# Kernel optimization log

Hardware: AMD Instinct MI355X
Metric: run time of the kernel (lower is better)

Reference implementation:

```python
import jax, jax.numpy as jnp
import numpy as np

N, E, F_IN, HID, HEADS, G = 50000, 800000, 128, 128, 4, 512
NEG_SLOPE = 0.2


def setup_inputs() -> dict:
    key = jax.random.key(0)
    ks = jax.random.split(key, 16)
    x = jax.random.normal(ks[0], (N, F_IN), dtype=jnp.float32)
    edge_index = jax.random.randint(ks[1], (2, E), 0, N, dtype=jnp.int32)
    batch = jnp.sort(jax.random.randint(ks[2], (N,), 0, G, dtype=jnp.int32))
    s1 = 1.0 / np.sqrt(F_IN)
    s2 = 1.0 / np.sqrt(HEADS * HID)
    params = {
        "W1": jax.random.uniform(ks[3], (F_IN, HEADS * HID), jnp.float32, -s1, s1),
        "a_src1": jax.random.normal(ks[4], (HEADS, HID), jnp.float32) * s1,
        "a_dst1": jax.random.normal(ks[5], (HEADS, HID), jnp.float32) * s1,
        "b1": jnp.zeros((HEADS * HID,), jnp.float32),
        "W2": jax.random.uniform(ks[6], (HEADS * HID, HID), jnp.float32, -s2, s2),
        "a_src2": jax.random.normal(ks[7], (1, HID), jnp.float32) * s2,
        "a_dst2": jax.random.normal(ks[8], (1, HID), jnp.float32) * s2,
        "b2": jnp.zeros((HID,), jnp.float32),
        "Wl": jax.random.normal(ks[9], (HID, 1), jnp.float32) / np.sqrt(HID),
        "bl": jnp.zeros((1,), jnp.float32),
    }
    return dict(x=x, edge_index=edge_index, batch=batch, **params)


def _gat_conv(x, W, a_src, a_dst, b, src, dst, heads, out_ch):
    n = x.shape[0]
    h = (x @ W).reshape(n, heads, out_ch)                      # [N,H,C]
    asrc = jnp.sum(h * a_src, axis=-1)                          # [N,H]
    adst = jnp.sum(h * a_dst, axis=-1)                          # [N,H]
    logits = jax.nn.leaky_relu(asrc[src] + adst[dst], NEG_SLOPE)  # [E,H]
    m = jax.ops.segment_max(logits, dst, num_segments=n)        # stable softmax per dst
    e = jnp.exp(logits - m[dst])
    denom = jax.ops.segment_sum(e, dst, num_segments=n)
    alpha = e / denom[dst]                                      # [E,H]
    out = jax.ops.segment_sum(alpha[:, :, None] * h[src], dst, num_segments=n)
    return out.reshape(n, heads * out_ch) + b


def reference(x, edge_index, batch, W1, a_src1, a_dst1, b1, W2, a_src2, a_dst2, b2, Wl, bl):
    n = x.shape[0]
    loop = jnp.arange(n, dtype=edge_index.dtype)
    src = jnp.concatenate([edge_index[0], loop])  # add_self_loops=True (PyG default)
    dst = jnp.concatenate([edge_index[1], loop])
    h = _gat_conv(x, W1, a_src1, a_dst1, b1, src, dst, HEADS, HID)
    h = jax.nn.elu(h)
    h = _gat_conv(h, W2, a_src2, a_dst2, b2, src, dst, 1, HID)
    h = jax.nn.elu(h)
    # global_mean_pool
    sums = jax.ops.segment_sum(h, batch, num_segments=G)
    cnts = jax.ops.segment_sum(jnp.ones((n,), h.dtype), batch, num_segments=G)
    pooled = sums / jnp.maximum(cnts, 1.0)[:, None]
    return (pooled @ Wl + bl).squeeze()
```

## Files before the change

kernel.cpp:

```cpp
#include <hip/hip_runtime.h>
#include <math.h>

#define NEG_SLOPE 0.2f

typedef float f4 __attribute__((ext_vector_type(4)));
typedef __attribute__((ext_vector_type(8))) short short8;
typedef __attribute__((ext_vector_type(4))) float f32x4;
typedef unsigned short ushort_t;

__device__ __forceinline__ float bf2f(unsigned short s) {
    unsigned u = ((unsigned)s) << 16;
    float f; __builtin_memcpy(&f, &u, 4); return f;
}
__device__ __forceinline__ unsigned short f2bf(float f) {
    unsigned u; __builtin_memcpy(&u, &f, 4);
    u = (u + 0x7FFFu + ((u >> 16) & 1u)) >> 16;
    return (unsigned short)u;
}
__device__ __forceinline__ void gload16(const void* g, void* l) {
    __builtin_amdgcn_global_load_lds((const __attribute__((address_space(1))) void*)g,
                                     (__attribute__((address_space(3))) void*)l, 16, 0, 0);
}

__global__ void hist_kernel(const int* __restrict__ ei, int E, int Et, int* __restrict__ deg) {
    int e = blockIdx.x * blockDim.x + threadIdx.x;
    if (e >= Et) return;
    int d = (e < E) ? ei[E + e] : (e - E);
    atomicAdd(&deg[d], 1);
}

__global__ __launch_bounds__(1024) void scan_local(const int* __restrict__ deg,
                                                   int* __restrict__ off,
                                                   int* __restrict__ btot, int n) {
    __shared__ int s_w[16];
    int tid = threadIdx.x, lane = tid & 63, wv = tid >> 6;
    int i = blockIdx.x * 1024 + tid;
    int v = (i < n) ? deg[i] : 0;
    int x = v;
    #pragma unroll
    for (int d = 1; d < 64; d <<= 1) {
        int y = __shfl_up(x, d);
        if (lane >= d) x += y;
    }
    if (lane == 63) s_w[wv] = x;
    __syncthreads();
    if (tid < 16) {
        int y = s_w[tid];
        int z = y;
        #pragma unroll
        for (int d = 1; d < 16; d <<= 1) {
            int t2 = __shfl_up(z, d);
            if (tid >= d) z += t2;
        }
        if (tid == 15) btot[blockIdx.x] = z;
        s_w[tid] = z - y;
    }
    __syncthreads();
    if (i < n) off[i] = s_w[wv] + (x - v);
}

__global__ void scan_base(int* __restrict__ btot, int nb) {
    int lane = threadIdx.x;
    int v = (lane < nb) ? btot[lane] : 0;
    int x = v;
    #pragma unroll
    for (int d = 1; d < 64; d <<= 1) {
        int y = __shfl_up(x, d);
        if (lane >= d) x += y;
    }
    int total = __shfl(x, nb - 1);
    if (lane < nb) btot[lane] = x - v;
    if (lane == 0) btot[nb] = total;
}

__global__ void scan_add(const int* __restrict__ btot, int* __restrict__ off,
                         int* __restrict__ cur, const int* __restrict__ batch,
                         int* __restrict__ gcnt, int n, int nb) {
    int i = blockIdx.x * blockDim.x + threadIdx.x;
    if (i < n) {
        int o = off[i] + btot[i >> 10];
        off[i] = o;
        cur[i] = o;
        atomicAdd(&gcnt[batch[i]], 1);
    } else if (i == n) {
        off[n] = btot[nb];
    }
}

__global__ void scatter_kernel(const int* __restrict__ ei, int E, int Et,
                               int* __restrict__ cur, int* __restrict__ csr) {
    int e = blockIdx.x * blockDim.x + threadIdx.x;
    if (e >= Et) return;
    int s, d;
    if (e < E) { s = ei[e]; d = ei[E + e]; }
    else       { s = d = e - E; }
    int p = atomicAdd(&cur[d], 1);
    csr[p] = s;
}

__global__ void cast_all(const float* __restrict__ x, const float* __restrict__ W1,
                         const float* __restrict__ W2, ushort_t* __restrict__ xb,
                         ushort_t* __restrict__ W1t, ushort_t* __restrict__ W2t,
                         int n_x, int pad_x) {
    int i = blockIdx.x * blockDim.x + threadIdx.x;
    if (i < pad_x) {
        xb[i] = f2bf(i < n_x ? x[i] : 0.f);
        return;
    }
    int k = i - pad_x;
    if (k < 128 * 512) {
        int r = k >> 9, c = k & 511;
        W1t[(size_t)c * 128 + r] = f2bf(W1[k]);
        return;
    }
    k -= 128 * 512;
    if (k < 512 * 128) {
        int r = k >> 7, c = k & 127;
        W2t[(size_t)c * 512 + r] = f2bf(W2[k]);
    }
}

template<int MI, int H>
__global__ __launch_bounds__(256) void gemm_bf16(const ushort_t* __restrict__ A,
                                                 const ushort_t* __restrict__ Bt,
                                                 ushort_t* __restrict__ C,
                                                 const float* __restrict__ aw_src,
                                                 const float* __restrict__ aw_dst,
                                                 float* __restrict__ avs,
                                                 float* __restrict__ avd,
                                                 int K, int Nc) {
    constexpr int BM = MI * 32;
    constexpr int AI = MI / 2;
    __shared__ __align__(16) ushort_t As[BM * 32];
    __shared__ __align__(16) ushort_t Bs[128 * 32];
    __shared__ __align__(16) ushort_t Cs[4 * MI * 16 * 72];
    const int t = threadIdx.x, w = t >> 6, lane = t & 63;
    const int r0 = blockIdx.x * BM, c0 = blockIdx.y * 128;
    const int wr = w & 1, wc = w >> 1;

    const ushort_t* Ag = A + (size_t)(r0 + w * (BM / 4) + (lane >> 2)) * K + (lane & 3) * 8;
    const ushort_t* Bg = Bt + (size_t)(c0 + w * 32 + (lane >> 2)) * K + (lane & 3) * 8;
    ushort_t* Al = As + w * (BM / 4) * 32;
    ushort_t* Bl = Bs + w * 1024;

    f32x4 acc[MI][4] = {};
    for (int k0 = 0; k0 < K; k0 += 32) {
        __syncthreads();
        #pragma unroll
        for (int m = 0; m < AI; m++) gload16(Ag + k0 + (size_t)m * 16 * K, Al + m * 512);
        gload16(Bg + k0, Bl);
        gload16(Bg + k0 + (size_t)16 * K, Bl + 512);
        __syncthreads();
        short8 af[MI], bf[4];
        #pragma unroll
        for (int i = 0; i < MI; i++)
            af[i] = *(const short8*)(As + (wr * MI * 16 + i * 16 + (lane & 15)) * 32 + (lane >> 4) * 8);
        #pragma unroll
        for (int jj = 0; jj < 4; jj++)
            bf[jj] = *(const short8*)(Bs + (wc * 64 + jj * 16 + (lane & 15)) * 32 + (lane >> 4) * 8);
        #pragma unroll
        for (int i = 0; i < MI; i++)
            #pragma unroll
            for (int jj = 0; jj < 4; jj++)
                acc[i][jj] = __builtin_amdgcn_mfma_f32_16x16x32_bf16(af[i], bf[jj], acc[i][jj], 0, 0, 0);
    }

    const int head = c0 >> 7;
    float asc[4], adc[4];
    #pragma unroll
    for (int jj = 0; jj < 4; jj++) {
        int c = c0 + wc * 64 + jj * 16 + (lane & 15);
        asc[jj] = aw_src[c];
        adc[jj] = aw_dst[c];
    }
    #pragma unroll
    for (int i = 0; i < MI; i++) {
        #pragma unroll
        for (int r = 0; r < 4; r++) {
            float ps = 0.f, pd = 0.f;
            #pragma unroll
            for (int jj = 0; jj < 4; jj++) {
                float v = acc[i][jj][r];
                ps = fmaf(v, asc[jj], ps);
                pd = fmaf(v, adc[jj], pd);
            }
            #pragma unroll
            for (int d = 1; d < 16; d <<= 1) {
                ps += __shfl_xor(ps, d);
                pd += __shfl_xor(pd, d);
            }
            if ((lane & 15) == 0) {
                int row = r0 + wr * MI * 16 + i * 16 + (lane >> 4) * 4 + r;
                atomicAdd(&avs[(size_t)row * H + head], ps);
                atomicAdd(&avd[(size_t)row * H + head], pd);
            }
        }
    }

    ushort_t* Cw = Cs + w * (MI * 16 * 72);
    #pragma unroll
    for (int i = 0; i < MI; i++)
        #pragma unroll
        for (int jj = 0; jj < 4; jj++)
            #pragma unroll
            for (int r = 0; r < 4; r++)
                Cw[(i * 16 + (lane >> 4) * 4 + r) * 72 + jj * 16 + (lane & 15)] = f2bf(acc[i][jj][r]);
    asm volatile("s_waitcnt lgkmcnt(0)" ::: "memory");
    #pragma unroll
    for (int pass = 0; pass < MI * 2; pass++) {
        int row_l = pass * 8 + (lane >> 3);
        short8 v = *(const short8*)(Cw + row_l * 72 + (lane & 7) * 8);
        int grow = r0 + wr * MI * 16 + row_l;
        int gcol = c0 + wc * 64 + (lane & 7) * 8;
        *(short8*)(C + (size_t)grow * Nc + gcol) = v;
    }
}

template<int H, int TOT, bool OUT_BF16>
__global__ __launch_bounds__(256) void agg_kernel(const int* __restrict__ off,
                                                  const int* __restrict__ csr,
                                                  const ushort_t* __restrict__ feat,
                                                  const float* __restrict__ avs,
                                                  const float* __restrict__ avd,
                                                  const float* __restrict__ bias,
                                                  void* __restrict__ outv, int n) {
    constexpr int J = TOT / 64;
    __shared__ float s_ex[4][64 * H];
    __shared__ int   s_sv[4][64];
    int w = threadIdx.x >> 6, lane = threadIdx.x & 63;
    int dst = blockIdx.x * 4 + w;
    if (dst >= n) return;
    const int h_own = (lane * J) / (TOT / H);
    float adv[H];
    if constexpr (H == 4) {
        f4 t4 = *(const f4*)&avd[(size_t)dst * 4];
        #pragma unroll
        for (int h = 0; h < 4; h++) adv[h] = t4[h];
    } else {
        adv[0] = avd[dst];
    }
    int beg = off[dst], end = off[dst + 1];
    float den = 0.f;
    float acc[J] = {};
    float* exw = s_ex[w];
    int*   svw = s_sv[w];

    for (int b = beg; b < end; b += 64) {
        int idx = b + lane;
        bool val = idx < end;
        int sv = val ? csr[idx] : 0;
        svw[lane] = sv;
        if constexpr (H == 4) {
            f4 av = {};
            if (val) av = *(const f4*)&avs[(size_t)sv * 4];
            f4 exv;
            #pragma unroll
            for (int h = 0; h < 4; h++) {
                float l = av[h] + adv[h];
                l = l > 0.f ? l : NEG_SLOPE * l;
                exv[h] = val ? __expf(l) : 0.f;
            }
            *(f4*)&exw[lane * 4] = exv;
        } else {
            float l = (val ? avs[sv] : 0.f) + adv[0];
            l = l > 0.f ? l : NEG_SLOPE * l;
            exw[lane] = val ? __expf(l) : 0.f;
        }
        asm volatile("s_waitcnt lgkmcnt(0)" ::: "memory");
        int cnt = min(64, end - b);
        int j = 0;
        for (; j + 2 <= cnt; j += 2) {
            int   s0 = svw[j],              s1 = svw[j + 1];
            float e0 = exw[j * H + h_own],  e1 = exw[(j + 1) * H + h_own];
            den += e0 + e1;
            const ushort_t* f0 = feat + (size_t)s0 * TOT + lane * J;
            const ushort_t* f1 = feat + (size_t)s1 * TOT + lane * J;
            if constexpr (J == 8) {
                short8 v0 = *(const short8*)f0;
                short8 v1 = *(const short8*)f1;
                #pragma unroll
                for (int u = 0; u < 8; u++) acc[u] += e0 * bf2f((unsigned short)v0[u]);
                #pragma unroll
                for (int u = 0; u < 8; u++) acc[u] += e1 * bf2f((unsigned short)v1[u]);
            } else {
                unsigned v0 = *(const unsigned*)f0;
                unsigned v1 = *(const unsigned*)f1;
                acc[0] += e0 * bf2f((unsigned short)(v0 & 0xffffu));
                acc[1] += e0 * bf2f((unsigned short)(v0 >> 16));
                acc[0] += e1 * bf2f((unsigned short)(v1 & 0xffffu));
                acc[1] += e1 * bf2f((unsigned short)(v1 >> 16));
            }
        }
        if (j < cnt) {
            int   s0 = svw[j];
            float e0 = exw[j * H + h_own];
            den += e0;
            const ushort_t* f0 = feat + (size_t)s0 * TOT + lane * J;
            if constexpr (J == 8) {
                short8 v0 = *(const short8*)f0;
                #pragma unroll
                for (int u = 0; u < 8; u++) acc[u] += e0 * bf2f((unsigned short)v0[u]);
            } else {
                unsigned v0 = *(const unsigned*)f0;
                acc[0] += e0 * bf2f((unsigned short)(v0 & 0xffffu));
                acc[1] += e0 * bf2f((unsigned short)(v0 >> 16));
            }
        }
    }
    float rden = 1.f / den;
    if constexpr (OUT_BF16) {
        unsigned short ov[J];
        #pragma unroll
        for (int u = 0; u < J; u++) {
            float v = acc[u] * rden + bias[lane * J + u];
            v = v > 0.f ? v : expm1f(v);
            ov[u] = f2bf(v);
        }
        *(short8*)((ushort_t*)outv + (size_t)dst * TOT + lane * J) = *(short8*)ov;
    } else {
        float v0 = acc[0] * rden + bias[lane * 2];
        float v1 = acc[1] * rden + bias[lane * 2 + 1];
        v0 = v0 > 0.f ? v0 : expm1f(v0);
        v1 = v1 > 0.f ? v1 : expm1f(v1);
        float2 vv = make_float2(v0, v1);
        *(float2*)((float*)outv + (size_t)dst * TOT + lane * 2) = vv;
    }
}

__global__ __launch_bounds__(256) void pool_kernel(const float* __restrict__ feat,
                                                   const int* __restrict__ batch,
                                                   float* __restrict__ gsum, int n) {
    int t = threadIdx.x;
    int ch = t & 127, half = t >> 7;
    int base = blockIdx.x * 64;
    float acc = 0.f;
    int curg = -1;
    for (int k = half; k < 64; k += 2) {
        int node = base + k;
        if (node >= n) break;
        int g = batch[node];
        if (g != curg) {
            if (curg >= 0) atomicAdd(&gsum[(size_t)curg * 128 + ch], acc);
            acc = 0.f;
            curg = g;
        }
        acc += feat[(size_t)node * 128 + ch];
    }
    if (curg >= 0) atomicAdd(&gsum[(size_t)curg * 128 + ch], acc);
}

__global__ __launch_bounds__(256) void final_kernel(const float* __restrict__ gsum,
                                                    const int* __restrict__ gcnt,
                                                    const float* __restrict__ Wl,
                                                    const float* __restrict__ bl,
                                                    float* __restrict__ out, int g_total) {
    int w = threadIdx.x >> 6, lane = threadIdx.x & 63;
    int g = blockIdx.x * 4 + w;
    if (g >= g_total) return;
    float inv = 1.f / fmaxf((float)gcnt[g], 1.f);
    float p = 0.f;
    #pragma unroll
    for (int j = 0; j < 2; j++) {
        int ch = lane + 64 * j;
        p += gsum[(size_t)g * 128 + ch] * Wl[ch];
    }
    #pragma unroll
    for (int d = 32; d; d >>= 1) p += __shfl_xor(p, d);
    if (lane == 0) out[g] = p * inv + bl[0];
}

extern "C" void kernel_launch(void* const* d_in, const int* in_sizes, int n_in,
                              void* d_out, int out_size, void* d_ws, size_t ws_size,
                              hipStream_t stream) {
    const float* x   = (const float*)d_in[0];
    const int*   ei  = (const int*)d_in[1];
    const int*   bat = (const int*)d_in[2];
    const float* W1  = (const float*)d_in[3];
    const float* as1 = (const float*)d_in[4];
    const float* ad1 = (const float*)d_in[5];
    const float* b1  = (const float*)d_in[6];
    const float* W2  = (const float*)d_in[7];
    const float* as2 = (const float*)d_in[8];
    const float* ad2 = (const float*)d_in[9];
    const float* b2  = (const float*)d_in[10];
    const float* Wl  = (const float*)d_in[11];
    const float* bl  = (const float*)d_in[12];
    float* out = (float*)d_out;

    const int N    = in_sizes[0] / 128;
    const int E    = in_sizes[1] / 2;
    const int Et   = E + N;
    const int G    = 512;
    const int Mpad = (N + 127) & ~127;
    const int nb   = (N + 1023) >> 10;

    char* p = (char*)d_ws;
    auto alloc = [&](size_t bytes) { char* r = p; p += (bytes + 255) & ~(size_t)255; return r; };
    ushort_t* xb    = (ushort_t*)alloc((size_t)Mpad * 128 * 2);
    ushort_t* W1t   = (ushort_t*)alloc((size_t)512 * 128 * 2);
    ushort_t* W2t   = (ushort_t*)alloc((size_t)128 * 512 * 2);
    ushort_t* h1b   = (ushort_t*)alloc((size_t)Mpad * 512 * 2);
    ushort_t* hb    = (ushort_t*)alloc((size_t)Mpad * 512 * 2);
    ushort_t* h2b   = (ushort_t*)alloc((size_t)Mpad * 128 * 2);
    float*    feat2 = (float*)alloc((size_t)N * 128 * 4);
    float*    avs1  = (float*)alloc((size_t)Mpad * 4 * 4);
    float*    avd1  = (float*)alloc((size_t)Mpad * 4 * 4);
    float*    avs2  = (float*)alloc((size_t)Mpad * 4);
    float*    avd2  = (float*)alloc((size_t)Mpad * 4);
    float*    gsum  = (float*)alloc((size_t)G * 128 * 4);
    int*      gcnt  = (int*)alloc((size_t)G * 4);
    int*      deg   = (int*)alloc((size_t)N * 4);
    int*      off   = (int*)alloc((size_t)(N + 1) * 4);
    int*      cur   = (int*)alloc((size_t)N * 4);
    int*      btot  = (int*)alloc((size_t)64 * 4);
    int*      csr   = (int*)alloc((size_t)Et * 4);

    hipMemsetAsync(avs1, 0, (size_t)((char*)off - (char*)avs1), stream);
    hipMemsetAsync(hb + (size_t)N * 512, 0, (size_t)(Mpad - N) * 512 * 2, stream);

    hist_kernel<<<(Et + 255) / 256, 256, 0, stream>>>(ei, E, Et, deg);
    scan_local<<<nb, 1024, 0, stream>>>(deg, off, btot, N);
    scan_base<<<1, 64, 0, stream>>>(btot, nb);
    scan_add<<<(N + 256) / 256, 256, 0, stream>>>(btot, off, cur, bat, gcnt, N, nb);
    cast_all<<<((Mpad * 128 + 2 * 65536) + 255) / 256, 256, 0, stream>>>(x, W1, W2, xb, W1t, W2t,
                                                                         N * 128, Mpad * 128);
    scatter_kernel<<<(Et + 255) / 256, 256, 0, stream>>>(ei, E, Et, cur, csr);

    gemm_bf16<4, 4><<<dim3(Mpad / 128, 4), 256, 0, stream>>>(xb, W1t, h1b, as1, ad1, avs1, avd1, 128, 512);
    agg_kernel<4, 512, true><<<(N + 3) / 4, 256, 0, stream>>>(off, csr, h1b, avs1, avd1, b1, hb, N);

    gemm_bf16<2, 1><<<dim3(Mpad / 64, 1), 256, 0, stream>>>(hb, W2t, h2b, as2, ad2, avs2, avd2, 512, 128);
    agg_kernel<1, 128, false><<<(N + 3) / 4, 256, 0, stream>>>(off, csr, h2b, avs2, avd2, b2, feat2, N);

    pool_kernel<<<(N + 63) / 64, 256, 0, stream>>>(feat2, bat, gsum, N);
    final_kernel<<<(G + 3) / 4, 256, 0, stream>>>(gsum, gcnt, Wl, bl, out, G);
}
```

Before: 501.6 us.

## Quantize GEMM outputs to per-row int8 and aggregate from quantized features

The GEMMs now compute full output rows per block and quantize each row to 8-bit with a per-row scale, writing uint8 features plus a scale array in place of bf16. The aggregation kernels gather these bytes, fold the row scale into the attention weight and correct the zero-point offset with a running sum. This halves the gather traffic in the edge-bound aggregation steps, and the attention-vector atomics become plain stores. The cost is lower feature precision, which risks accuracy tolerance, plus a different GEMM tiling with smaller row tiles.

New measurement: 441.7 us. 11.9% less time.

```diff
diff --git a/kernel.cpp b/kernel.cpp
--- a/kernel.cpp
+++ b/kernel.cpp
@@ -7,6 +7,7 @@
 typedef __attribute__((ext_vector_type(8))) short short8;
 typedef __attribute__((ext_vector_type(4))) float f32x4;
 typedef unsigned short ushort_t;
+typedef unsigned char uchar_t;
 
 __device__ __forceinline__ float bf2f(unsigned short s) {
     unsigned u = ((unsigned)s) << 16;
@@ -120,66 +121,89 @@
     }
 }
 
-template<int MI, int H>
-__global__ __launch_bounds__(256) void gemm_bf16(const ushort_t* __restrict__ A,
-                                                 const ushort_t* __restrict__ Bt,
-                                                 ushort_t* __restrict__ C,
-                                                 const float* __restrict__ aw_src,
-                                                 const float* __restrict__ aw_dst,
-                                                 float* __restrict__ avs,
-                                                 float* __restrict__ avd,
-                                                 int K, int Nc) {
-    constexpr int BM = MI * 32;
-    constexpr int AI = MI / 2;
-    __shared__ __align__(16) ushort_t As[BM * 32];
-    __shared__ __align__(16) ushort_t Bs[128 * 32];
-    __shared__ __align__(16) ushort_t Cs[4 * MI * 16 * 72];
+template<int BN, int H>
+__global__ __launch_bounds__(256) void gemm_q(const ushort_t* __restrict__ A,
+                                              const ushort_t* __restrict__ Bt,
+                                              uchar_t* __restrict__ Cq,
+                                              float* __restrict__ Csc,
+                                              const float* __restrict__ aw_src,
+                                              const float* __restrict__ aw_dst,
+                                              float* __restrict__ avs,
+                                              float* __restrict__ avd,
+                                              int K) {
+    constexpr int CT = BN / 64;
+    __shared__ __align__(16) ushort_t As[32 * 32];
+    __shared__ __align__(16) ushort_t Bs[BN * 32];
+    __shared__ float s_rm[4][32];
+    __shared__ float s_rs[32];
+    __shared__ float s_avp[2][4][32];
     const int t = threadIdx.x, w = t >> 6, lane = t & 63;
-    const int r0 = blockIdx.x * BM, c0 = blockIdx.y * 128;
-    const int wr = w & 1, wc = w >> 1;
-
-    const ushort_t* Ag = A + (size_t)(r0 + w * (BM / 4) + (lane >> 2)) * K + (lane & 3) * 8;
-    const ushort_t* Bg = Bt + (size_t)(c0 + w * 32 + (lane >> 2)) * K + (lane & 3) * 8;
-    ushort_t* Al = As + w * (BM / 4) * 32;
-    ushort_t* Bl = Bs + w * 1024;
-
-    f32x4 acc[MI][4] = {};
+    const int r0 = blockIdx.x * 32;
+
+    const ushort_t* Ag = A + (size_t)(r0 + w * 16 + (lane >> 2)) * K + (lane & 3) * 8;
+    const ushort_t* Bg = Bt + (size_t)(w * (BN / 4) + (lane >> 2)) * K + (lane & 3) * 8;
+    ushort_t* Al = As + w * 512;
+    ushort_t* Bl = Bs + w * (BN / 4) * 32;
+
+    f32x4 acc[2][CT] = {};
     for (int k0 = 0; k0 < K; k0 += 32) {
         __syncthreads();
-        #pragma unroll
-        for (int m = 0; m < AI; m++) gload16(Ag + k0 + (size_t)m * 16 * K, Al + m * 512);
-        gload16(Bg + k0, Bl);
-        gload16(Bg + k0 + (size_t)16 * K, Bl + 512);
+        if (w < 2) gload16(Ag + k0, Al);
+        #pragma unroll
+        for (int m = 0; m < CT; m++)
+            gload16(Bg + k0 + (size_t)m * 16 * K, Bl + m * 512);
         __syncthreads();
-        short8 af[MI], bf[4];
-        #pragma unroll
-        for (int i = 0; i < MI; i++)
-            af[i] = *(const short8*)(As + (wr * MI * 16 + i * 16 + (lane & 15)) * 32 + (lane >> 4) * 8);
-        #pragma unroll
-        for (int jj = 0; jj < 4; jj++)
-            bf[jj] = *(const short8*)(Bs + (wc * 64 + jj * 16 + (lane & 15)) * 32 + (lane >> 4) * 8);
-        #pragma unroll
-        for (int i = 0; i < MI; i++)
-            #pragma unroll
-            for (int jj = 0; jj < 4; jj++)
+        short8 af[2], bf[CT];
+        #pragma unroll
+        for (int i = 0; i < 2; i++)
+            af[i] = *(const short8*)(As + (i * 16 + (lane & 15)) * 32 + (lane >> 4) * 8);
+        #pragma unroll
+        for (int jj = 0; jj < CT; jj++)
+            bf[jj] = *(const short8*)(Bs + (w * (BN / 4) + jj * 16 + (lane & 15)) * 32 + (lane >> 4) * 8);
+        #pragma unroll
+        for (int i = 0; i < 2; i++)
+            #pragma unroll
+            for (int jj = 0; jj < CT; jj++)
                 acc[i][jj] = __builtin_amdgcn_mfma_f32_16x16x32_bf16(af[i], bf[jj], acc[i][jj], 0, 0, 0);
     }
 
-    const int head = c0 >> 7;
-    float asc[4], adc[4];
-    #pragma unroll
-    for (int jj = 0; jj < 4; jj++) {
-        int c = c0 + wc * 64 + jj * 16 + (lane & 15);
+    float mr[2][4];
+    #pragma unroll
+    for (int i = 0; i < 2; i++)
+        #pragma unroll
+        for (int r = 0; r < 4; r++) {
+            float m = 0.f;
+            #pragma unroll
+            for (int jj = 0; jj < CT; jj++) m = fmaxf(m, fabsf(acc[i][jj][r]));
+            mr[i][r] = m;
+        }
+    #pragma unroll
+    for (int d = 1; d < 16; d <<= 1)
+        #pragma unroll
+        for (int i = 0; i < 2; i++)
+            #pragma unroll
+            for (int r = 0; r < 4; r++) mr[i][r] = fmaxf(mr[i][r], __shfl_xor(mr[i][r], d));
+    if ((lane & 15) == 0) {
+        #pragma unroll
+        for (int i = 0; i < 2; i++)
+            #pragma unroll
+            for (int r = 0; r < 4; r++) s_rm[w][i * 16 + (lane >> 4) * 4 + r] = mr[i][r];
+    }
+
+    float asc[CT], adc[CT];
+    #pragma unroll
+    for (int jj = 0; jj < CT; jj++) {
+        int c = w * (BN / 4) + jj * 16 + (lane & 15);
         asc[jj] = aw_src[c];
         adc[jj] = aw_dst[c];
     }
     #pragma unroll
-    for (int i = 0; i < MI; i++) {
+    for (int i = 0; i < 2; i++) {
         #pragma unroll
         for (int r = 0; r < 4; r++) {
             float ps = 0.f, pd = 0.f;
             #pragma unroll
-            for (int jj = 0; jj < 4; jj++) {
+            for (int jj = 0; jj < CT; jj++) {
                 float v = acc[i][jj][r];
                 ps = fmaf(v, asc[jj], ps);
                 pd = fmaf(v, adc[jj], pd);
@@ -190,47 +214,69 @@
                 pd += __shfl_xor(pd, d);
             }
             if ((lane & 15) == 0) {
-                int row = r0 + wr * MI * 16 + i * 16 + (lane >> 4) * 4 + r;
-                atomicAdd(&avs[(size_t)row * H + head], ps);
-                atomicAdd(&avd[(size_t)row * H + head], pd);
-            }
-        }
-    }
-
-    ushort_t* Cw = Cs + w * (MI * 16 * 72);
-    #pragma unroll
-    for (int i = 0; i < MI; i++)
-        #pragma unroll
-        for (int jj = 0; jj < 4; jj++)
-            #pragma unroll
-            for (int r = 0; r < 4; r++)
-                Cw[(i * 16 + (lane >> 4) * 4 + r) * 72 + jj * 16 + (lane & 15)] = f2bf(acc[i][jj][r]);
-    asm volatile("s_waitcnt lgkmcnt(0)" ::: "memory");
-    #pragma unroll
-    for (int pass = 0; pass < MI * 2; pass++) {
-        int row_l = pass * 8 + (lane >> 3);
-        short8 v = *(const short8*)(Cw + row_l * 72 + (lane & 7) * 8);
-        int grow = r0 + wr * MI * 16 + row_l;
-        int gcol = c0 + wc * 64 + (lane & 7) * 8;
-        *(short8*)(C + (size_t)grow * Nc + gcol) = v;
+                int row = i * 16 + (lane >> 4) * 4 + r;
+                if constexpr (H == 4) {
+                    avs[(size_t)(r0 + row) * 4 + w] = ps;
+                    avd[(size_t)(r0 + row) * 4 + w] = pd;
+                } else {
+                    s_avp[0][w][row] = ps;
+                    s_avp[1][w][row] = pd;
+                }
+            }
+        }
+    }
+    __syncthreads();
+    if (t < 32) {
+        float rm = fmaxf(fmaxf(s_rm[0][t], s_rm[1][t]), fmaxf(s_rm[2][t], s_rm[3][t]));
+        rm = fmaxf(rm, 1e-30f);
+        Csc[r0 + t] = rm * (1.f / 127.f);
+        s_rs[t] = 127.f / rm;
+        if constexpr (H == 1) {
+            avs[r0 + t] = s_avp[0][0][t] + s_avp[0][1][t] + s_avp[0][2][t] + s_avp[0][3][t];
+            avd[r0 + t] = s_avp[1][0][t] + s_avp[1][1][t] + s_avp[1][2][t] + s_avp[1][3][t];
+        }
+    }
+    __syncthreads();
+    uchar_t* s_q = (uchar_t*)Bs;
+    #pragma unroll
+    for (int i = 0; i < 2; i++)
+        #pragma unroll
+        for (int jj = 0; jj < CT; jj++)
+            #pragma unroll
+            for (int r = 0; r < 4; r++) {
+                int row = i * 16 + (lane >> 4) * 4 + r;
+                int col = w * (BN / 4) + jj * 16 + (lane & 15);
+                int qi = (int)rintf(acc[i][jj][r] * s_rs[row]) + 128;
+                qi = min(255, max(0, qi));
+                s_q[row * BN + col] = (uchar_t)qi;
+            }
+    __syncthreads();
+    constexpr int PASSES = BN / 128;
+    constexpr int CPR = BN / 16;
+    #pragma unroll
+    for (int p2 = 0; p2 < PASSES; p2++) {
+        int idx = p2 * 256 + t;
+        int row = idx / CPR, ch = idx % CPR;
+        *(uint4*)(Cq + (size_t)(r0 + row) * BN + ch * 16) =
+            *(const uint4*)(s_q + row * BN + ch * 16);
     }
 }
 
 template<int H, int TOT, bool OUT_BF16>
-__global__ __launch_bounds__(256) void agg_kernel(const int* __restrict__ off,
-                                                  const int* __restrict__ csr,
-                                                  const ushort_t* __restrict__ feat,
-                                                  const float* __restrict__ avs,
-                                                  const float* __restrict__ avd,
-                                                  const float* __restrict__ bias,
-                                                  void* __restrict__ outv, int n) {
+__global__ __launch_bounds__(256) void agg_q(const int* __restrict__ off,
+                                             const int* __restrict__ csr,
+                                             const uchar_t* __restrict__ fq,
+                                             const float* __restrict__ fs,
+                                             const float* __restrict__ avs,
+                                             const float* __restrict__ avd,
+                                             const float* __restrict__ bias,
+                                             void* __restrict__ outv, int n) {
     constexpr int J = TOT / 64;
     __shared__ float s_ex[4][64 * H];
-    __shared__ int   s_sv[4][64];
     int w = threadIdx.x >> 6, lane = threadIdx.x & 63;
     int dst = blockIdx.x * 4 + w;
     if (dst >= n) return;
-    const int h_own = (lane * J) / (TOT / H);
+    const int h_own = (H == 1) ? 0 : (lane >> 4);
     float adv[H];
     if constexpr (H == 4) {
         f4 t4 = *(const f4*)&avd[(size_t)dst * 4];
@@ -240,86 +286,123 @@
         adv[0] = avd[dst];
     }
     int beg = off[dst], end = off[dst + 1];
-    float den = 0.f;
+    float den[H] = {}, Ssum[H] = {};
     float acc[J] = {};
     float* exw = s_ex[w];
-    int*   svw = s_sv[w];
 
     for (int b = beg; b < end; b += 64) {
         int idx = b + lane;
         bool val = idx < end;
         int sv = val ? csr[idx] : 0;
-        svw[lane] = sv;
+        float srow = fs[sv];
+        unsigned myoff = (unsigned)sv * TOT;
         if constexpr (H == 4) {
-            f4 av = {};
-            if (val) av = *(const f4*)&avs[(size_t)sv * 4];
+            f4 av = *(const f4*)&avs[(size_t)sv * 4];
             f4 exv;
             #pragma unroll
             for (int h = 0; h < 4; h++) {
                 float l = av[h] + adv[h];
-                l = l > 0.f ? l : NEG_SLOPE * l;
-                exv[h] = val ? __expf(l) : 0.f;
+                l = fmaxf(l, l * NEG_SLOPE);
+                float e = val ? __expf(l) : 0.f;
+                den[h] += e;
+                float es = e * srow;
+                Ssum[h] += es;
+                exv[h] = es;
             }
             *(f4*)&exw[lane * 4] = exv;
         } else {
-            float l = (val ? avs[sv] : 0.f) + adv[0];
-            l = l > 0.f ? l : NEG_SLOPE * l;
-            exw[lane] = val ? __expf(l) : 0.f;
+            float l = avs[sv] + adv[0];
+            l = fmaxf(l, l * NEG_SLOPE);
+            float e = val ? __expf(l) : 0.f;
+            den[0] += e;
+            float es = e * srow;
+            Ssum[0] += es;
+            exw[lane] = es;
         }
         asm volatile("s_waitcnt lgkmcnt(0)" ::: "memory");
         int cnt = min(64, end - b);
         int j = 0;
         for (; j + 2 <= cnt; j += 2) {
-            int   s0 = svw[j],              s1 = svw[j + 1];
-            float e0 = exw[j * H + h_own],  e1 = exw[(j + 1) * H + h_own];
-            den += e0 + e1;
-            const ushort_t* f0 = feat + (size_t)s0 * TOT + lane * J;
-            const ushort_t* f1 = feat + (size_t)s1 * TOT + lane * J;
+            float e0 = exw[j * H + h_own];
+            float e1 = exw[(j + 1) * H + h_own];
+            unsigned v0 = (unsigned)__shfl((int)myoff, j) + lane * J;
+            unsigned v1 = (unsigned)__shfl((int)myoff, j + 1) + lane * J;
             if constexpr (J == 8) {
-                short8 v0 = *(const short8*)f0;
-                short8 v1 = *(const short8*)f1;
-                #pragma unroll
-                for (int u = 0; u < 8; u++) acc[u] += e0 * bf2f((unsigned short)v0[u]);
-                #pragma unroll
-                for (int u = 0; u < 8; u++) acc[u] += e1 * bf2f((unsigned short)v1[u]);
+                uint2 u0 = *(const uint2*)(fq + v0);
+                uint2 u1 = *(const uint2*)(fq + v1);
+                acc[0] += e0 * (float)(u0.x & 0xffu);
+                acc[1] += e0 * (float)((u0.x >> 8) & 0xffu);
+                acc[2] += e0 * (float)((u0.x >> 16) & 0xffu);
+                acc[3] += e0 * (float)(u0.x >> 24);
+                acc[4] += e0 * (float)(u0.y & 0xffu);
+                acc[5] += e0 * (float)((u0.y >> 8) & 0xffu);
+                acc[6] += e0 * (float)((u0.y >> 16) & 0xffu);
+                acc[7] += e0 * (float)(u0.y >> 24);
+                acc[0] += e1 * (float)(u1.x & 0xffu);
+                acc[1] += e1 * (float)((u1.x >> 8) & 0xffu);
+                acc[2] += e1 * (float)((u1.x >> 16) & 0xffu);
+                acc[3] += e1 * (float)(u1.x >> 24);
+                acc[4] += e1 * (float)(u1.y & 0xffu);
+                acc[5] += e1 * (float)((u1.y >> 8) & 0xffu);
+                acc[6] += e1 * (float)((u1.y >> 16) & 0xffu);
+                acc[7] += e1 * (float)(u1.y >> 24);
             } else {
-                unsigned v0 = *(const unsigned*)f0;
-                unsigned v1 = *(const unsigned*)f1;
-                acc[0] += e0 * bf2f((unsigned short)(v0 & 0xffffu));
-                acc[1] += e0 * bf2f((unsigned short)(v0 >> 16));
-                acc[0] += e1 * bf2f((unsigned short)(v1 & 0xffffu));
-                acc[1] += e1 * bf2f((unsigned short)(v1 >> 16));
+                unsigned us0 = *(const ushort_t*)(fq + v0);
+                unsigned us1 = *(const ushort_t*)(fq + v1);
+                acc[0] += e0 * (float)(us0 & 0xffu);
+                acc[1] += e0 * (float)(us0 >> 8);
+                acc[0] += e1 * (float)(us1 & 0xffu);
+                acc[1] += e1 * (float)(us1 >> 8);
             }
         }
         if (j < cnt) {
-            int   s0 = svw[j];
             float e0 = exw[j * H + h_own];
-            den += e0;
-            const ushort_t* f0 = feat + (size_t)s0 * TOT + lane * J;
+            unsigned v0 = (unsigned)__shfl((int)myoff, j) + lane * J;
             if constexpr (J == 8) {
-                short8 v0 = *(const short8*)f0;
-                #pragma unroll
-                for (int u = 0; u < 8; u++) acc[u] += e0 * bf2f((unsigned short)v0[u]);
+                uint2 u0 = *(const uint2*)(fq + v0);
+                acc[0] += e0 * (float)(u0.x & 0xffu);
+                acc[1] += e0 * (float)((u0.x >> 8) & 0xffu);
+                acc[2] += e0 * (float)((u0.x >> 16) & 0xffu);
+                acc[3] += e0 * (float)(u0.x >> 24);
+                acc[4] += e0 * (float)(u0.y & 0xffu);
+                acc[5] += e0 * (float)((u0.y >> 8) & 0xffu);
+                acc[6] += e0 * (float)((u0.y >> 16) & 0xffu);
+                acc[7] += e0 * (float)(u0.y >> 24);
             } else {
-                unsigned v0 = *(const unsigned*)f0;
-                acc[0] += e0 * bf2f((unsigned short)(v0 & 0xffffu));
-                acc[1] += e0 * bf2f((unsigned short)(v0 >> 16));
-            }
-        }
-    }
-    float rden = 1.f / den;
+                unsigned us0 = *(const ushort_t*)(fq + v0);
+                acc[0] += e0 * (float)(us0 & 0xffu);
+                acc[1] += e0 * (float)(us0 >> 8);
+            }
+        }
+    }
+    #pragma unroll
+    for (int h = 0; h < H; h++) {
+        #pragma unroll
+        for (int d = 32; d; d >>= 1) {
+            den[h] += __shfl_xor(den[h], d);
+            Ssum[h] += __shfl_xor(Ssum[h], d);
+        }
+    }
+    float dh, Sh;
+    if constexpr (H == 4) {
+        dh = (lane & 32) ? ((lane & 16) ? den[3] : den[2]) : ((lane & 16) ? den[1] : den[0]);
+        Sh = (lane & 32) ? ((lane & 16) ? Ssum[3] : Ssum[2]) : ((lane & 16) ? Ssum[1] : Ssum[0]);
+    } else {
+        dh = den[0]; Sh = Ssum[0];
+    }
+    float rden = 1.f / dh;
     if constexpr (OUT_BF16) {
         unsigned short ov[J];
         #pragma unroll
         for (int u = 0; u < J; u++) {
-            float v = acc[u] * rden + bias[lane * J + u];
+            float v = (acc[u] - 128.f * Sh) * rden + bias[lane * J + u];
             v = v > 0.f ? v : expm1f(v);
             ov[u] = f2bf(v);
         }
         *(short8*)((ushort_t*)outv + (size_t)dst * TOT + lane * J) = *(short8*)ov;
     } else {
-        float v0 = acc[0] * rden + bias[lane * 2];
-        float v1 = acc[1] * rden + bias[lane * 2 + 1];
+        float v0 = (acc[0] - 128.f * Sh) * rden + bias[lane * 2];
+        float v1 = (acc[1] - 128.f * Sh) * rden + bias[lane * 2 + 1];
         v0 = v0 > 0.f ? v0 : expm1f(v0);
         v1 = v1 > 0.f ? v1 : expm1f(v1);
         float2 vv = make_float2(v0, v1);
@@ -399,9 +482,11 @@
     ushort_t* xb    = (ushort_t*)alloc((size_t)Mpad * 128 * 2);
     ushort_t* W1t   = (ushort_t*)alloc((size_t)512 * 128 * 2);
     ushort_t* W2t   = (ushort_t*)alloc((size_t)128 * 512 * 2);
-    ushort_t* h1b   = (ushort_t*)alloc((size_t)Mpad * 512 * 2);
+    uchar_t*  h1q   = (uchar_t*)alloc((size_t)Mpad * 512);
+    float*    h1s   = (float*)alloc((size_t)Mpad * 4);
     ushort_t* hb    = (ushort_t*)alloc((size_t)Mpad * 512 * 2);
-    ushort_t* h2b   = (ushort_t*)alloc((size_t)Mpad * 128 * 2);
+    uchar_t*  h2q   = (uchar_t*)alloc((size_t)Mpad * 128);
+    float*    h2s   = (float*)alloc((size_t)Mpad * 4);
     float*    feat2 = (float*)alloc((size_t)N * 128 * 4);
     float*    avs1  = (float*)alloc((size_t)Mpad * 4 * 4);
     float*    avd1  = (float*)alloc((size_t)Mpad * 4 * 4);
@@ -412,10 +497,10 @@
     int*      deg   = (int*)alloc((size_t)N * 4);
     int*      off   = (int*)alloc((size_t)(N + 1) * 4);
     int*      cur   = (int*)alloc((size_t)N * 4);
-    int*      btot  = (int*)alloc((size_t)64 * 4);
+    int*      btot  = (int*)alloc((size_t)128 * 4);
     int*      csr   = (int*)alloc((size_t)Et * 4);
 
-    hipMemsetAsync(avs1, 0, (size_t)((char*)off - (char*)avs1), stream);
+    hipMemsetAsync(gsum, 0, (size_t)((char*)off - (char*)gsum), stream);
     hipMemsetAsync(hb + (size_t)N * 512, 0, (size_t)(Mpad - N) * 512 * 2, stream);
 
     hist_kernel<<<(Et + 255) / 256, 256, 0, stream>>>(ei, E, Et, deg);
@@ -426,11 +511,11 @@
                                                                          N * 128, Mpad * 128);
     scatter_kernel<<<(Et + 255) / 256, 256, 0, stream>>>(ei, E, Et, cur, csr);
 
-    gemm_bf16<4, 4><<<dim3(Mpad / 128, 4), 256, 0, stream>>>(xb, W1t, h1b, as1, ad1, avs1, avd1, 128, 512);
-    agg_kernel<4, 512, true><<<(N + 3) / 4, 256, 0, stream>>>(off, csr, h1b, avs1, avd1, b1, hb, N);
-
-    gemm_bf16<2, 1><<<dim3(Mpad / 64, 1), 256, 0, stream>>>(hb, W2t, h2b, as2, ad2, avs2, avd2, 512, 128);
-    agg_kernel<1, 128, false><<<(N + 3) / 4, 256, 0, stream>>>(off, csr, h2b, avs2, avd2, b2, feat2, N);
+    gemm_q<512, 4><<<Mpad / 32, 256, 0, stream>>>(xb, W1t, h1q, h1s, as1, ad1, avs1, avd1, 128);
+    agg_q<4, 512, true><<<(N + 3) / 4, 256, 0, stream>>>(off, csr, h1q, h1s, avs1, avd1, b1, hb, N);
+
+    gemm_q<128, 1><<<Mpad / 32, 256, 0, stream>>>(hb, W2t, h2q, h2s, as2, ad2, avs2, avd2, 512);
+    agg_q<1, 128, false><<<(N + 3) / 4, 256, 0, stream>>>(off, csr, h2q, h2s, avs2, avd2, b2, feat2, N);
 
     pool_kernel<<<(N + 63) / 64, 256, 0, stream>>>(feat2, bat, gsum, N);
     final_kernel<<<(G + 3) / 4, 256, 0, stream>>>(gsum, gcnt, Wl, bl, out, G);
```
